# Kernel tuning notes

Measured on AMD Instinct MI355X. Metric: run time of the kernel, lower is better.

Reference implementation:

```python
import jax, jax.numpy as jnp
import numpy as np

BS, NS, NM, NO = 262144, 16, 8, 8

def setup_inputs() -> dict:
    key = jax.random.key(0)
    k = jax.random.split(key, 6)
    z = jax.random.normal(k[0], (BS, NM), dtype=jnp.float32)
    x0 = jax.random.normal(k[1], (BS, NS), dtype=jnp.float32)
    A = jax.random.normal(k[2], (BS, NS, NS), dtype=jnp.float32) * 0.1
    # PSD initial covariance per batch element
    P0 = jnp.einsum('bij,bkj->bik', A, A) + jnp.eye(NS, dtype=jnp.float32)
    phi = jnp.eye(NS, dtype=jnp.float32) + 0.01 * jax.random.normal(k[3], (NS, NS), dtype=jnp.float32)
    H = jax.random.normal(k[4], (NM, NS), dtype=jnp.float32) * 0.3
    C = jax.random.normal(k[5], (NO, NS), dtype=jnp.float32) * 0.3
    Qdiag = jnp.full((NS,), 0.1, dtype=jnp.float32)
    Rdiag = jnp.full((NM,), 0.1, dtype=jnp.float32)
    return {"z": z, "x0": x0, "P0": P0, "phi": phi, "H": H, "C": C,
            "Qdiag": Qdiag, "Rdiag": Rdiag}

def reference(z, x0, P0, phi, H, C, Qdiag, Rdiag):
    # --- predict ---
    x_pred = x0 @ phi.T                                       # [bs, ns]
    P_pred = jnp.einsum('ij,bjk,lk->bil', phi, P0, phi) + jnp.diag(Qdiag)  # phi P phi^T + Q
    # --- innovation ---
    y = z - x_pred @ H.T                                      # [bs, nm]
    S = jnp.einsum('ij,bjk,lk->bil', H, P_pred, H) + jnp.diag(Rdiag)       # H P H^T + R
    Sinv = jnp.linalg.inv(S)                                  # [bs, nm, nm]
    # --- gain and update ---
    K = jnp.einsum('bij,kj,bkl->bil', P_pred, H, Sinv)        # P H^T S^-1 [bs, ns, nm]
    x_new = x_pred + jnp.einsum('bij,bj->bi', K, y)           # [bs, ns]
    P_new = P_pred - jnp.einsum('bij,jk,bkl->bil', K, H, P_pred)  # (I - K H) P
    out = x_new @ C.T                                         # [bs, no]
    return out
```

## Files before the change

kernel.cpp:

```cpp
#include <hip/hip_runtime.h>


#define QFMA(ACC, OFF, A, V) { ACC[(OFF)+0] += (A)*(V).x; ACC[(OFF)+1] += (A)*(V).y; ACC[(OFF)+2] += (A)*(V).z; ACC[(OFF)+3] += (A)*(V).w; }
#define TS 132

__global__ __launch_bounds__(256) void kalman_fused5(
    const float* __restrict__ z,
    const float* __restrict__ x0,
    const float* __restrict__ P0,
    const float* __restrict__ phi,
    const float* __restrict__ Hm,
    const float* __restrict__ Cm,
    const float* __restrict__ Qd,
    const float* __restrict__ Rd,
    float* __restrict__ out,
    int bs)
{
    __shared__ __align__(16) float phiS[16 * 20];
    __shared__ __align__(16) float HnS[8 * 20];
    __shared__ __align__(16) float CsS[8 * 20];
    __shared__ __align__(16) float BnS[8 * 20];
    __shared__ __align__(16) float BTS[16 * 8];
    __shared__ __align__(16) float CpS[8 * 20];
    __shared__ __align__(16) float CQHS[8 * 8];
    __shared__ __align__(16) float ScS[8 * 8];
    __shared__            float QdS[16];
    __shared__            float RdS[8];
    __shared__ __align__(16) float x0S[32 * 20];
    __shared__ __align__(16) float Tb[32 * TS];

    const int tid = threadIdx.x;
    const int e = tid >> 3;
    const int i = tid & 7;
    long b = (long)blockIdx.x * 32 + e;
    const bool valid = (b < (long)bs);
    if (!valid) b = (long)bs - 1;

    {
        const int r = tid >> 4, c = tid & 15;
        phiS[r * 20 + c] = phi[tid];
    }
    if (tid < 128) {
        const int m = tid >> 4, k = tid & 15;
        HnS[m * 20 + k] = Hm[tid];
        CsS[m * 20 + k] = Cm[tid];
    }
    if (tid < 16) QdS[tid] = Qd[tid];
    if (tid < 8)  RdS[tid] = Rd[tid];

    const float x0a = x0[b * 16 + i];
    const float x0b = x0[b * 16 + 8 + i];
    x0S[e * 20 + i]     = x0a;
    x0S[e * 20 + i + 8] = x0b;
    float yv = z[b * 8 + i];
    float4 Pq[8];
    {
        const float4* P0v = reinterpret_cast<const float4*>(P0 + (size_t)b * 256);
#pragma unroll
        for (int q = 0; q < 4; ++q) {
            Pq[q]     = P0v[i * 4 + q];
            Pq[q + 4] = P0v[(i + 8) * 4 + q];
        }
    }
    __syncthreads();

    if (tid < 128) {
        const int m = tid >> 4, k = tid & 15;
        float bv = 0.f, cv = 0.f;
#pragma unroll
        for (int j = 0; j < 16; ++j) {
            const float pj = phiS[j * 20 + k];
            bv += HnS[m * 20 + j] * pj;
            cv += CsS[m * 20 + j] * pj;
        }
        BnS[m * 20 + k] = bv;
        BTS[k * 8 + m]  = bv;
        CpS[m * 20 + k] = cv;
    }
    if (tid < 64) {
        const int i2 = tid >> 3, j2 = tid & 7;
        float sc = (i2 == j2) ? RdS[i2] : 0.f;
        float cq = 0.f;
#pragma unroll
        for (int k = 0; k < 16; ++k) {
            const float qh = QdS[k] * HnS[j2 * 20 + k];
            sc += HnS[i2 * 20 + k] * qh;
            cq += CsS[i2 * 20 + k] * qh;
        }
        ScS[i2 * 8 + j2]  = sc;
        CQHS[i2 * 8 + j2] = cq;
    }
    __syncthreads();

    float t0[8], t1[8];
#pragma unroll
    for (int m = 0; m < 8; ++m) { t0[m] = 0.f; t1[m] = 0.f; }
#pragma unroll
    for (int q = 0; q < 4; ++q) {
        const float4 A = Pq[q], B4 = Pq[q + 4];
        const float a[4] = {A.x, A.y, A.z, A.w};
        const float c[4] = {B4.x, B4.y, B4.z, B4.w};
#pragma unroll
        for (int kk = 0; kk < 4; ++kk) {
            const int k = 4 * q + kk;
            const float4 b0 = *reinterpret_cast<const float4*>(&BTS[k * 8 + 0]);
            const float4 b1 = *reinterpret_cast<const float4*>(&BTS[k * 8 + 4]);
            QFMA(t0, 0, a[kk], b0) QFMA(t0, 4, a[kk], b1)
            QFMA(t1, 0, c[kk], b0) QFMA(t1, 4, c[kk], b1)
        }
    }
    *reinterpret_cast<float4*>(&Tb[e * TS + i * 8 + 0]) = make_float4(t0[0], t0[1], t0[2], t0[3]);
    *reinterpret_cast<float4*>(&Tb[e * TS + i * 8 + 4]) = make_float4(t0[4], t0[5], t0[6], t0[7]);
    *reinterpret_cast<float4*>(&Tb[e * TS + (i + 8) * 8 + 0]) = make_float4(t1[0], t1[1], t1[2], t1[3]);
    *reinterpret_cast<float4*>(&Tb[e * TS + (i + 8) * 8 + 4]) = make_float4(t1[4], t1[5], t1[6], t1[7]);

    float br[16];
#pragma unroll
    for (int q = 0; q < 4; ++q) {
        const float4 A = *reinterpret_cast<const float4*>(&BnS[i * 20 + 4 * q]);
        br[4*q+0] = A.x; br[4*q+1] = A.y; br[4*q+2] = A.z; br[4*q+3] = A.w;
    }

    float s[8];
    {
        const float4 c0 = *reinterpret_cast<const float4*>(&ScS[i * 8 + 0]);
        const float4 c1 = *reinterpret_cast<const float4*>(&ScS[i * 8 + 4]);
        s[0]=c0.x; s[1]=c0.y; s[2]=c0.z; s[3]=c0.w; s[4]=c1.x; s[5]=c1.y; s[6]=c1.z; s[7]=c1.w;
    }
#pragma unroll
    for (int j = 0; j < 16; ++j) {
        const float4 ta = *reinterpret_cast<const float4*>(&Tb[e * TS + j * 8 + 0]);
        const float4 tb = *reinterpret_cast<const float4*>(&Tb[e * TS + j * 8 + 4]);
        const float bij = br[j];
        QFMA(s, 0, bij, ta) QFMA(s, 4, bij, tb)
    }

#pragma unroll
    for (int q = 0; q < 4; ++q) {
        const float4 X = *reinterpret_cast<const float4*>(&x0S[e * 20 + 4 * q]);
        yv -= br[4*q+0]*X.x + br[4*q+1]*X.y + br[4*q+2]*X.z + br[4*q+3]*X.w;
    }

#pragma unroll
    for (int k = 0; k < 7; ++k) {
        float pr[8];
#pragma unroll
        for (int j = k; j < 8; ++j) pr[j] = __shfl(s[j], k, 8);
        const float py = __shfl(yv, k, 8);
        if (i > k) {
            const float f = s[k] / pr[k];
#pragma unroll
            for (int j = k; j < 8; ++j) s[j] -= f * pr[j];
            yv -= f * py;
        }
    }
    float w[8];
#pragma unroll
    for (int k = 7; k >= 0; --k) {
        const float num = __shfl(yv, k, 8);
        const float den = __shfl(s[k], k, 8);
        const float wk = num / den;
        w[k] = wk;
        if (i < k) yv -= s[k] * wk;
    }

    float th0 = 0.f, th1 = 0.f;
#pragma unroll
    for (int m = 0; m < 8; ++m) { th0 += t0[m] * w[m]; th1 += t1[m] * w[m]; }
    const float u0v = x0a + th0;
    const float u1v = x0b + th1;

    float uv[16];
#pragma unroll
    for (int j = 0; j < 8; ++j) {
        uv[j]     = __shfl(u0v, j, 8);
        uv[j + 8] = __shfl(u1v, j, 8);
    }

    float oc = 0.f;
#pragma unroll
    for (int q = 0; q < 4; ++q) {
        const float4 A = *reinterpret_cast<const float4*>(&CpS[i * 20 + 4 * q]);
        oc += A.x*uv[4*q+0] + A.y*uv[4*q+1] + A.z*uv[4*q+2] + A.w*uv[4*q+3];
    }
    {
        const float4 q0 = *reinterpret_cast<const float4*>(&CQHS[i * 8 + 0]);
        const float4 q1 = *reinterpret_cast<const float4*>(&CQHS[i * 8 + 4]);
        oc += q0.x*w[0] + q0.y*w[1] + q0.z*w[2] + q0.w*w[3]
            + q1.x*w[4] + q1.y*w[5] + q1.z*w[6] + q1.w*w[7];
    }
    if (valid) out[b * 8 + i] = oc;
}

extern "C" void kernel_launch(void* const* d_in, const int* in_sizes, int n_in,
                              void* d_out, int out_size, void* d_ws, size_t ws_size,
                              hipStream_t stream)
{
    const float* z   = (const float*)d_in[0];
    const float* x0  = (const float*)d_in[1];
    const float* P0  = (const float*)d_in[2];
    const float* phi = (const float*)d_in[3];
    const float* H   = (const float*)d_in[4];
    const float* C   = (const float*)d_in[5];
    const float* Qd  = (const float*)d_in[6];
    const float* Rd  = (const float*)d_in[7];
    float* out = (float*)d_out;

    const int bs = in_sizes[0] / 8;
    const int blocks = (bs + 31) / 32;
    hipLaunchKernelGGL(kalman_fused5, dim3(blocks), dim3(256), 0, stream,
                       z, x0, P0, phi, H, C, Qd, Rd, out, bs);
}
```

Before: 80.04 us.

## Convert Kalman kernel to persistent grid-stride loop with capped block count

The launch now caps the grid at 1536 blocks, and each block loops over 32-element batch chunks. Per-block setup (B=H·phi, C·phi, S constant, C·Q·H^T) is computed once per block and reused across iterations, reading phi, H and C straight from global memory instead of staging them in shared memory first. This spreads the constant-matrix setup and its barriers over several chunks. The trade-off is that P0 loads are no longer issued ahead of a barrier, so fewer independent loads may be in flight per CU on this bandwidth-heavy workload.

New measurement: 83.05 us. +3.8%, slower.

```diff
diff --git a/kernel.cpp b/kernel.cpp
--- a/kernel.cpp
+++ b/kernel.cpp
@@ -4,7 +4,7 @@
 #define QFMA(ACC, OFF, A, V) { ACC[(OFF)+0] += (A)*(V).x; ACC[(OFF)+1] += (A)*(V).y; ACC[(OFF)+2] += (A)*(V).z; ACC[(OFF)+3] += (A)*(V).w; }
 #define TS 132
 
-__global__ __launch_bounds__(256) void kalman_fused5(
+__global__ __launch_bounds__(256) void kalman_fused6(
     const float* __restrict__ z,
     const float* __restrict__ x0,
     const float* __restrict__ P0,
@@ -16,62 +16,26 @@
     float* __restrict__ out,
     int bs)
 {
-    __shared__ __align__(16) float phiS[16 * 20];
-    __shared__ __align__(16) float HnS[8 * 20];
-    __shared__ __align__(16) float CsS[8 * 20];
     __shared__ __align__(16) float BnS[8 * 20];
     __shared__ __align__(16) float BTS[16 * 8];
     __shared__ __align__(16) float CpS[8 * 20];
     __shared__ __align__(16) float CQHS[8 * 8];
     __shared__ __align__(16) float ScS[8 * 8];
-    __shared__            float QdS[16];
-    __shared__            float RdS[8];
     __shared__ __align__(16) float x0S[32 * 20];
     __shared__ __align__(16) float Tb[32 * TS];
 
     const int tid = threadIdx.x;
     const int e = tid >> 3;
     const int i = tid & 7;
-    long b = (long)blockIdx.x * 32 + e;
-    const bool valid = (b < (long)bs);
-    if (!valid) b = (long)bs - 1;
-
-    {
-        const int r = tid >> 4, c = tid & 15;
-        phiS[r * 20 + c] = phi[tid];
-    }
-    if (tid < 128) {
-        const int m = tid >> 4, k = tid & 15;
-        HnS[m * 20 + k] = Hm[tid];
-        CsS[m * 20 + k] = Cm[tid];
-    }
-    if (tid < 16) QdS[tid] = Qd[tid];
-    if (tid < 8)  RdS[tid] = Rd[tid];
-
-    const float x0a = x0[b * 16 + i];
-    const float x0b = x0[b * 16 + 8 + i];
-    x0S[e * 20 + i]     = x0a;
-    x0S[e * 20 + i + 8] = x0b;
-    float yv = z[b * 8 + i];
-    float4 Pq[8];
-    {
-        const float4* P0v = reinterpret_cast<const float4*>(P0 + (size_t)b * 256);
-#pragma unroll
-        for (int q = 0; q < 4; ++q) {
-            Pq[q]     = P0v[i * 4 + q];
-            Pq[q + 4] = P0v[(i + 8) * 4 + q];
-        }
-    }
-    __syncthreads();
 
     if (tid < 128) {
         const int m = tid >> 4, k = tid & 15;
         float bv = 0.f, cv = 0.f;
 #pragma unroll
         for (int j = 0; j < 16; ++j) {
-            const float pj = phiS[j * 20 + k];
-            bv += HnS[m * 20 + j] * pj;
-            cv += CsS[m * 20 + j] * pj;
+            const float pj = phi[j * 16 + k];
+            bv += Hm[m * 16 + j] * pj;
+            cv += Cm[m * 16 + j] * pj;
         }
         BnS[m * 20 + k] = bv;
         BTS[k * 8 + m]  = bv;
@@ -79,117 +43,139 @@
     }
     if (tid < 64) {
         const int i2 = tid >> 3, j2 = tid & 7;
-        float sc = (i2 == j2) ? RdS[i2] : 0.f;
+        float sc = (i2 == j2) ? Rd[i2] : 0.f;
         float cq = 0.f;
 #pragma unroll
         for (int k = 0; k < 16; ++k) {
-            const float qh = QdS[k] * HnS[j2 * 20 + k];
-            sc += HnS[i2 * 20 + k] * qh;
-            cq += CsS[i2 * 20 + k] * qh;
+            const float qh = Qd[k] * Hm[j2 * 16 + k];
+            sc += Hm[i2 * 16 + k] * qh;
+            cq += Cm[i2 * 16 + k] * qh;
         }
         ScS[i2 * 8 + j2]  = sc;
         CQHS[i2 * 8 + j2] = cq;
     }
     __syncthreads();
 
-    float t0[8], t1[8];
-#pragma unroll
-    for (int m = 0; m < 8; ++m) { t0[m] = 0.f; t1[m] = 0.f; }
-#pragma unroll
-    for (int q = 0; q < 4; ++q) {
-        const float4 A = Pq[q], B4 = Pq[q + 4];
-        const float a[4] = {A.x, A.y, A.z, A.w};
-        const float c[4] = {B4.x, B4.y, B4.z, B4.w};
-#pragma unroll
-        for (int kk = 0; kk < 4; ++kk) {
-            const int k = 4 * q + kk;
-            const float4 b0 = *reinterpret_cast<const float4*>(&BTS[k * 8 + 0]);
-            const float4 b1 = *reinterpret_cast<const float4*>(&BTS[k * 8 + 4]);
-            QFMA(t0, 0, a[kk], b0) QFMA(t0, 4, a[kk], b1)
-            QFMA(t1, 0, c[kk], b0) QFMA(t1, 4, c[kk], b1)
-        }
+    const long stride = (long)gridDim.x * 32;
+#pragma unroll 1
+    for (long b0 = (long)blockIdx.x * 32; b0 < (long)bs; b0 += stride) {
+        const long b = b0 + e;
+        if (b >= (long)bs) continue;
+
+        float4 Pq[8];
+        {
+            const float4* P0v = reinterpret_cast<const float4*>(P0 + (size_t)b * 256);
+#pragma unroll
+            for (int q = 0; q < 4; ++q) {
+                Pq[q]     = P0v[i * 4 + q];
+                Pq[q + 4] = P0v[(i + 8) * 4 + q];
+            }
+        }
+        const float x0a = x0[b * 16 + i];
+        const float x0b = x0[b * 16 + 8 + i];
+        float yv = z[b * 8 + i];
+        x0S[e * 20 + i]     = x0a;
+        x0S[e * 20 + i + 8] = x0b;
+
+        float t0[8], t1[8];
+#pragma unroll
+        for (int m = 0; m < 8; ++m) { t0[m] = 0.f; t1[m] = 0.f; }
+#pragma unroll
+        for (int q = 0; q < 4; ++q) {
+            const float4 A = Pq[q], B4 = Pq[q + 4];
+            const float a[4] = {A.x, A.y, A.z, A.w};
+            const float c[4] = {B4.x, B4.y, B4.z, B4.w};
+#pragma unroll
+            for (int kk = 0; kk < 4; ++kk) {
+                const int k = 4 * q + kk;
+                const float4 b0v = *reinterpret_cast<const float4*>(&BTS[k * 8 + 0]);
+                const float4 b1v = *reinterpret_cast<const float4*>(&BTS[k * 8 + 4]);
+                QFMA(t0, 0, a[kk], b0v) QFMA(t0, 4, a[kk], b1v)
+                QFMA(t1, 0, c[kk], b0v) QFMA(t1, 4, c[kk], b1v)
+            }
+        }
+        *reinterpret_cast<float4*>(&Tb[e * TS + i * 8 + 0]) = make_float4(t0[0], t0[1], t0[2], t0[3]);
+        *reinterpret_cast<float4*>(&Tb[e * TS + i * 8 + 4]) = make_float4(t0[4], t0[5], t0[6], t0[7]);
+        *reinterpret_cast<float4*>(&Tb[e * TS + (i + 8) * 8 + 0]) = make_float4(t1[0], t1[1], t1[2], t1[3]);
+        *reinterpret_cast<float4*>(&Tb[e * TS + (i + 8) * 8 + 4]) = make_float4(t1[4], t1[5], t1[6], t1[7]);
+
+        float br[16];
+#pragma unroll
+        for (int q = 0; q < 4; ++q) {
+            const float4 A = *reinterpret_cast<const float4*>(&BnS[i * 20 + 4 * q]);
+            br[4*q+0] = A.x; br[4*q+1] = A.y; br[4*q+2] = A.z; br[4*q+3] = A.w;
+        }
+
+        float s[8];
+        {
+            const float4 c0 = *reinterpret_cast<const float4*>(&ScS[i * 8 + 0]);
+            const float4 c1 = *reinterpret_cast<const float4*>(&ScS[i * 8 + 4]);
+            s[0]=c0.x; s[1]=c0.y; s[2]=c0.z; s[3]=c0.w; s[4]=c1.x; s[5]=c1.y; s[6]=c1.z; s[7]=c1.w;
+        }
+#pragma unroll
+        for (int j = 0; j < 16; ++j) {
+            const float4 ta = *reinterpret_cast<const float4*>(&Tb[e * TS + j * 8 + 0]);
+            const float4 tb = *reinterpret_cast<const float4*>(&Tb[e * TS + j * 8 + 4]);
+            const float bij = br[j];
+            QFMA(s, 0, bij, ta) QFMA(s, 4, bij, tb)
+        }
+
+#pragma unroll
+        for (int q = 0; q < 4; ++q) {
+            const float4 X = *reinterpret_cast<const float4*>(&x0S[e * 20 + 4 * q]);
+            yv -= br[4*q+0]*X.x + br[4*q+1]*X.y + br[4*q+2]*X.z + br[4*q+3]*X.w;
+        }
+
+#pragma unroll
+        for (int k = 0; k < 7; ++k) {
+            float pr[8];
+#pragma unroll
+            for (int j = k; j < 8; ++j) pr[j] = __shfl(s[j], k, 8);
+            const float py = __shfl(yv, k, 8);
+            if (i > k) {
+                const float f = s[k] / pr[k];
+#pragma unroll
+                for (int j = k; j < 8; ++j) s[j] -= f * pr[j];
+                yv -= f * py;
+            }
+        }
+        float w[8];
+#pragma unroll
+        for (int k = 7; k >= 0; --k) {
+            const float num = __shfl(yv, k, 8);
+            const float den = __shfl(s[k], k, 8);
+            const float wk = num / den;
+            w[k] = wk;
+            if (i < k) yv -= s[k] * wk;
+        }
+
+        float th0 = 0.f, th1 = 0.f;
+#pragma unroll
+        for (int m = 0; m < 8; ++m) { th0 += t0[m] * w[m]; th1 += t1[m] * w[m]; }
+        const float u0v = x0a + th0;
+        const float u1v = x0b + th1;
+
+        float uv[16];
+#pragma unroll
+        for (int j = 0; j < 8; ++j) {
+            uv[j]     = __shfl(u0v, j, 8);
+            uv[j + 8] = __shfl(u1v, j, 8);
+        }
+
+        float oc = 0.f;
+#pragma unroll
+        for (int q = 0; q < 4; ++q) {
+            const float4 A = *reinterpret_cast<const float4*>(&CpS[i * 20 + 4 * q]);
+            oc += A.x*uv[4*q+0] + A.y*uv[4*q+1] + A.z*uv[4*q+2] + A.w*uv[4*q+3];
+        }
+        {
+            const float4 q0 = *reinterpret_cast<const float4*>(&CQHS[i * 8 + 0]);
+            const float4 q1 = *reinterpret_cast<const float4*>(&CQHS[i * 8 + 4]);
+            oc += q0.x*w[0] + q0.y*w[1] + q0.z*w[2] + q0.w*w[3]
+                + q1.x*w[4] + q1.y*w[5] + q1.z*w[6] + q1.w*w[7];
+        }
+        out[b * 8 + i] = oc;
     }
-    *reinterpret_cast<float4*>(&Tb[e * TS + i * 8 + 0]) = make_float4(t0[0], t0[1], t0[2], t0[3]);
-    *reinterpret_cast<float4*>(&Tb[e * TS + i * 8 + 4]) = make_float4(t0[4], t0[5], t0[6], t0[7]);
-    *reinterpret_cast<float4*>(&Tb[e * TS + (i + 8) * 8 + 0]) = make_float4(t1[0], t1[1], t1[2], t1[3]);
-    *reinterpret_cast<float4*>(&Tb[e * TS + (i + 8) * 8 + 4]) = make_float4(t1[4], t1[5], t1[6], t1[7]);
-
-    float br[16];
-#pragma unroll
-    for (int q = 0; q < 4; ++q) {
-        const float4 A = *reinterpret_cast<const float4*>(&BnS[i * 20 + 4 * q]);
-        br[4*q+0] = A.x; br[4*q+1] = A.y; br[4*q+2] = A.z; br[4*q+3] = A.w;
-    }
-
-    float s[8];
-    {
-        const float4 c0 = *reinterpret_cast<const float4*>(&ScS[i * 8 + 0]);
-        const float4 c1 = *reinterpret_cast<const float4*>(&ScS[i * 8 + 4]);
-        s[0]=c0.x; s[1]=c0.y; s[2]=c0.z; s[3]=c0.w; s[4]=c1.x; s[5]=c1.y; s[6]=c1.z; s[7]=c1.w;
-    }
-#pragma unroll
-    for (int j = 0; j < 16; ++j) {
-        const float4 ta = *reinterpret_cast<const float4*>(&Tb[e * TS + j * 8 + 0]);
-        const float4 tb = *reinterpret_cast<const float4*>(&Tb[e * TS + j * 8 + 4]);
-        const float bij = br[j];
-        QFMA(s, 0, bij, ta) QFMA(s, 4, bij, tb)
-    }
-
-#pragma unroll
-    for (int q = 0; q < 4; ++q) {
-        const float4 X = *reinterpret_cast<const float4*>(&x0S[e * 20 + 4 * q]);
-        yv -= br[4*q+0]*X.x + br[4*q+1]*X.y + br[4*q+2]*X.z + br[4*q+3]*X.w;
-    }
-
-#pragma unroll
-    for (int k = 0; k < 7; ++k) {
-        float pr[8];
-#pragma unroll
-        for (int j = k; j < 8; ++j) pr[j] = __shfl(s[j], k, 8);
-        const float py = __shfl(yv, k, 8);
-        if (i > k) {
-            const float f = s[k] / pr[k];
-#pragma unroll
-            for (int j = k; j < 8; ++j) s[j] -= f * pr[j];
-            yv -= f * py;
-        }
-    }
-    float w[8];
-#pragma unroll
-    for (int k = 7; k >= 0; --k) {
-        const float num = __shfl(yv, k, 8);
-        const float den = __shfl(s[k], k, 8);
-        const float wk = num / den;
-        w[k] = wk;
-        if (i < k) yv -= s[k] * wk;
-    }
-
-    float th0 = 0.f, th1 = 0.f;
-#pragma unroll
-    for (int m = 0; m < 8; ++m) { th0 += t0[m] * w[m]; th1 += t1[m] * w[m]; }
-    const float u0v = x0a + th0;
-    const float u1v = x0b + th1;
-
-    float uv[16];
-#pragma unroll
-    for (int j = 0; j < 8; ++j) {
-        uv[j]     = __shfl(u0v, j, 8);
-        uv[j + 8] = __shfl(u1v, j, 8);
-    }
-
-    float oc = 0.f;
-#pragma unroll
-    for (int q = 0; q < 4; ++q) {
-        const float4 A = *reinterpret_cast<const float4*>(&CpS[i * 20 + 4 * q]);
-        oc += A.x*uv[4*q+0] + A.y*uv[4*q+1] + A.z*uv[4*q+2] + A.w*uv[4*q+3];
-    }
-    {
-        const float4 q0 = *reinterpret_cast<const float4*>(&CQHS[i * 8 + 0]);
-        const float4 q1 = *reinterpret_cast<const float4*>(&CQHS[i * 8 + 4]);
-        oc += q0.x*w[0] + q0.y*w[1] + q0.z*w[2] + q0.w*w[3]
-            + q1.x*w[4] + q1.y*w[5] + q1.z*w[6] + q1.w*w[7];
-    }
-    if (valid) out[b * 8 + i] = oc;
 }
 
 extern "C" void kernel_launch(void* const* d_in, const int* in_sizes, int n_in,
@@ -207,7 +193,8 @@
     float* out = (float*)d_out;
 
     const int bs = in_sizes[0] / 8;
-    const int blocks = (bs + 31) / 32;
-    hipLaunchKernelGGL(kalman_fused5, dim3(blocks), dim3(256), 0, stream,
+    const int chunks = (bs + 31) / 32;
+    const int blocks = (chunks < 1536) ? chunks : 1536;
+    hipLaunchKernelGGL(kalman_fused6, dim3(blocks), dim3(256), 0, stream,
                        z, x0, P0, phi, H, C, Qd, Rd, out, bs);
 }
```
